# Kernel tuning notes

Measured on AMD Instinct MI355X. Metric: run time of the kernel, lower is better.

Reference implementation:

```python
import jax, jax.numpy as jnp
import numpy as np

ALPHA = 0.2        # LeakyReLU negative slope
OUT_FEATURE = 256
NEG_INF = -1e9


def setup_inputs() -> dict:
    key = jax.random.key(0)
    k1, k2, k3, k4 = jax.random.split(key, 4)
    N, F_IN, F_OUT = 8192, 512, OUT_FEATURE
    x = jax.random.normal(k1, (N, F_IN), dtype=jnp.float32)
    adj = jax.random.randint(k2, (N, N), 0, 2, dtype=jnp.int32)
    # Xavier-uniform-ish params
    W = jax.random.normal(k3, (F_IN, F_OUT), dtype=jnp.float32) * (1.414 / np.sqrt(F_IN))
    a = jax.random.normal(k4, (2 * F_OUT, 1), dtype=jnp.float32) * (1.414 / np.sqrt(2 * F_OUT))
    return {"x": x, "adj": adj, "W": W, "a": a}


def reference(x, adj, W, a):
    # x: [N, F_in], adj: [N, N] int, W: [F_in, F_out], a: [2*F_out, 1]
    h = x @ W                                   # [N, F_out]
    a_src = a[:OUT_FEATURE, 0]                  # [F_out]
    a_dst = a[OUT_FEATURE:, 0]                  # [F_out]
    e_i = h @ a_src                             # [N]
    e_j = h @ a_dst                             # [N]
    e = e_i[:, None] + e_j[None, :]             # [N, N] additive scores
    e = jnp.where(e > 0, e, ALPHA * e)          # LeakyReLU
    e = jnp.where(adj <= 0, NEG_INF, e)         # mask non-edges
    attn = jax.nn.softmax(e, axis=-1)           # row-wise softmax
    out = attn @ h                              # [N, F_out] aggregate
    return jax.nn.elu(out)                      # dropout is identity in eval
```

## Files before the change

### kernel.cpp

```cpp
#include <hip/hip_runtime.h>
#include <hip/hip_fp16.h>

#define N_NODES 8192
#define F_IN    512
#define F_OUT   256
#define LOG2E   1.4426950408889634f

typedef __attribute__((ext_vector_type(8))) _Float16 half8;
typedef __attribute__((ext_vector_type(2))) __fp16   fp16x2;
typedef __attribute__((ext_vector_type(4))) float    f32x4;
typedef __attribute__((ext_vector_type(4))) int      i32x4;

union H8U4 { half8 h; uint4 u; };
union H2U  { fp16x2 h; unsigned u; };

__global__ __launch_bounds__(256) void k_prep(const float* __restrict__ W,
                                              unsigned short* __restrict__ wph,
                                              unsigned short* __restrict__ wpl,
                                              unsigned* __restrict__ emax_u) {
  const int gid = blockIdx.x * 256 + threadIdx.x;
  if (gid == 0) *emax_u = 0u;
  const int k = gid >> 8;
  const int c = gid & 255;
  const float w = W[(size_t)k * F_OUT + c];
  const _Float16 hi = (_Float16)w;
  const _Float16 lo = (_Float16)(w - (float)hi);
  const size_t idx =
      (((size_t)(k >> 5) * 16 + (c >> 4)) * 64 + (c & 15) + 16 * ((k >> 3) & 3)) * 8 +
      (k & 7);
  wph[idx] = *(const unsigned short*)&hi;
  wpl[idx] = *(const unsigned short*)&lo;
}

__global__ __launch_bounds__(512) void k_hgemm(const float* __restrict__ x,
                                               const uint4* __restrict__ wph4,
                                               const uint4* __restrict__ wpl4,
                                               const float* __restrict__ a,
                                               unsigned short* __restrict__ hpack,
                                               float* __restrict__ EI,
                                               float* __restrict__ EJ,
                                               unsigned* __restrict__ emax_u) {
  __shared__ float eip[4][32], ejp[4][32], emx[32];
  const int r0   = blockIdx.x * 32;
  const int tid  = threadIdx.x;
  const int wid  = tid >> 6, lane = tid & 63;
  const int mg   = wid >> 2, ng = wid & 3;
  const int lo16 = lane & 15, hi4 = lane >> 4;

  const float* xrow = x + (size_t)(r0 + mg * 16 + lo16) * F_IN + hi4 * 8;
  const uint4* whb = wph4 + (size_t)(ng * 4) * 64 + lane;
  const uint4* wlb = wpl4 + (size_t)(ng * 4) * 64 + lane;

  f32x4 acc[4] = {};

  float4 xa = *(const float4*)(xrow);
  float4 xb = *(const float4*)(xrow + 4);
  uint4 wh[4], wl[4];
#pragma unroll
  for (int nf = 0; nf < 4; ++nf) {
    wh[nf] = whb[(size_t)nf * 64];
    wl[nf] = wlb[(size_t)nf * 64];
  }

#pragma unroll
  for (int ks = 0; ks < 16; ++ks) {
    H8U4 ah, al;
    const float v[8] = {xa.x, xa.y, xa.z, xa.w, xb.x, xb.y, xb.z, xb.w};
#pragma unroll
    for (int j = 0; j < 8; ++j) {
      const _Float16 h = (_Float16)v[j];
      ah.h[j] = h;
      al.h[j] = (_Float16)(v[j] - (float)h);
    }
    if (ks + 1 < 16) {
      xa = *(const float4*)(xrow + (ks + 1) * 32);
      xb = *(const float4*)(xrow + (ks + 1) * 32 + 4);
    }
#pragma unroll
    for (int nf = 0; nf < 4; ++nf) {
      H8U4 bh, bl;
      bh.u = wh[nf];
      bl.u = wl[nf];
      acc[nf] = __builtin_amdgcn_mfma_f32_16x16x32_f16(ah.h, bh.h, acc[nf], 0, 0, 0);
      acc[nf] = __builtin_amdgcn_mfma_f32_16x16x32_f16(al.h, bh.h, acc[nf], 0, 0, 0);
      acc[nf] = __builtin_amdgcn_mfma_f32_16x16x32_f16(ah.h, bl.h, acc[nf], 0, 0, 0);
    }
    if (ks + 1 < 16) {
#pragma unroll
      for (int nf = 0; nf < 4; ++nf) {
        wh[nf] = whb[(size_t)((ks + 1) * 16 + nf) * 64];
        wl[nf] = wlb[(size_t)((ks + 1) * 16 + nf) * 64];
      }
    }
  }

  float asv[4], adv[4];
#pragma unroll
  for (int nf = 0; nf < 4; ++nf) {
    const int c = ng * 64 + nf * 16 + lo16;
    asv[nf] = a[c];
    adv[nf] = a[F_OUT + c];
  }
#pragma unroll
  for (int q = 0; q < 4; ++q) {
    float s1 = acc[0][q] * asv[0] + acc[1][q] * asv[1] + acc[2][q] * asv[2] +
               acc[3][q] * asv[3];
    float s2 = acc[0][q] * adv[0] + acc[1][q] * adv[1] + acc[2][q] * adv[2] +
               acc[3][q] * adv[3];
#pragma unroll
    for (int o = 1; o < 16; o <<= 1) {
      s1 += __shfl_xor(s1, o);
      s2 += __shfl_xor(s2, o);
    }
    if (lo16 == 0) {
      const int rl = mg * 16 + hi4 * 4 + q;
      eip[ng][rl] = s1;
      ejp[ng][rl] = s2;
    }
  }

#pragma unroll
  for (int nf = 0; nf < 4; ++nf) {
#pragma unroll
    for (int q = 0; q < 4; ++q) {
      const int row = r0 + mg * 16 + hi4 * 4 + q;
      const int col = ng * 64 + nf * 16 + lo16;
      const size_t idx =
          (((size_t)(row >> 5) * 16 + (col >> 4)) * 64 + (col & 15) +
           16 * ((row >> 3) & 3)) * 8 + (row & 7);
      const _Float16 hv = (_Float16)acc[nf][q];
      hpack[idx] = *(const unsigned short*)&hv;
    }
  }

  __syncthreads();
  if (tid < 32) {
    const float s1 = eip[0][tid] + eip[1][tid] + eip[2][tid] + eip[3][tid];
    const float s2 = ejp[0][tid] + ejp[1][tid] + ejp[2][tid] + ejp[3][tid];
    const int row = r0 + tid;
    EI[row] = s1 * LOG2E;
    const float e2 = s2 * LOG2E;
    EJ[row] = e2;
    emx[tid] = e2;
  }
  __syncthreads();
  if (tid == 0) {
    float m = emx[0];
#pragma unroll
    for (int i = 1; i < 32; ++i) m = fmaxf(m, emx[i]);
    unsigned b = __float_as_uint(m);
    unsigned u = (b & 0x80000000u) ? ~b : (b | 0x80000000u);
    atomicMax(emax_u, u);
  }
}

__global__ __launch_bounds__(512, 4) void k_pv(const int* __restrict__ adj,
                                               const uint4* __restrict__ hp4,
                                               const float* __restrict__ EI,
                                               const float* __restrict__ EJ,
                                               const unsigned* __restrict__ emax_u,
                                               float* __restrict__ npart,
                                               float* __restrict__ dpart,
                                               int ntiles) {
  __shared__ __align__(16) uint4 ps4[8 * 64];
  __shared__ float ejhi[2048], ejlo[2048];
  __shared__ float A1[64], A2[64], den[64];
  __shared__ unsigned char bml[2][512];
  const int rowbase = blockIdx.x * 64;
  const int split   = blockIdx.y;
  const int jt0     = split * ntiles;
  const int tid     = threadIdx.x;
  const int wid  = tid >> 6, lane = tid & 63;
  const int lo   = lane & 15, hi = lane >> 4;

  float EMAX;
  {
    const unsigned u = *emax_u;
    EMAX = (u & 0x80000000u) ? __uint_as_float(u & 0x7fffffffu) : __uint_as_float(~u);
  }
  if (tid < 64) {
    const float e  = EI[rowbase + tid];
    const float s  = e + EMAX;
    const float mi = fmaxf(s, 0.2f * s);
    A1[tid] = e - mi;
    A2[tid] = 0.2f * e - mi;
    den[tid] = 0.f;
  }
  const bool uselds = (ntiles <= 32);
  if (uselds) {
    int eidx = jt0 * 64 + tid * 4;
    if (eidx > N_NODES - 4) eidx = N_NODES - 4;
    const float4 ev = *(const float4*)&EJ[eidx];
    *(float4*)&ejhi[tid * 4] = ev;
    float4 el = {0.2f * ev.x, 0.2f * ev.y, 0.2f * ev.z, 0.2f * ev.w};
    *(float4*)&ejlo[tid * 4] = el;
  }

  const int arow = tid >> 3;
  const int* aadj = adj + (size_t)(rowbase + arow) * N_NODES + jt0 * 64 + (tid & 7) * 8;
  {
    const i32x4 v0 = __builtin_nontemporal_load((const i32x4*)(aadj));
    const i32x4 v1 = __builtin_nontemporal_load((const i32x4*)(aadj + 4));
    unsigned by = (v0.x > 0) | ((v0.y > 0) << 1) | ((v0.z > 0) << 2) |
                  ((v0.w > 0) << 3) | ((v1.x > 0) << 4) | ((v1.y > 0) << 5) |
                  ((v1.z > 0) << 6) | ((v1.w > 0) << 7);
    bml[0][tid] = (unsigned char)by;
  }
  i32x4 av0 = {0, 0, 0, 0}, av1 = {0, 0, 0, 0};
  if (ntiles > 1) {
    av0 = __builtin_nontemporal_load((const i32x4*)(aadj + 64));
    av1 = __builtin_nontemporal_load((const i32x4*)(aadj + 68));
  }
  __syncthreads();

  const int msub = wid & 3, ksw = wid >> 2;
  const int row_p = msub * 16 + lo;
  const int jloc  = ksw * 32 + hi * 8;
  const float a1r = A1[row_p], a2r = A2[row_p];
  const int  mbidx = row_p * 8 + ksw * 4 + hi;
  const float* ejg  = EJ + jt0 * 64 + jloc;
  const int mg = wid >> 2, ng = wid & 3;
  const uint4* hb = hp4 + (ng * 4) * 64 + lane;

  f32x4 acc[2][4] = {};
  float dacc = 0.f;

  for (int jt = 0; jt < ntiles; ++jt) {
    const int tb = (jt0 + jt) * 2048;
    const uint4 b00 = hb[tb + 0 * 1024 + 0 * 64];
    const uint4 b01 = hb[tb + 0 * 1024 + 1 * 64];
    const uint4 b02 = hb[tb + 0 * 1024 + 2 * 64];
    const uint4 b03 = hb[tb + 0 * 1024 + 3 * 64];
    const uint4 b10 = hb[tb + 1 * 1024 + 0 * 64];
    const uint4 b11 = hb[tb + 1 * 1024 + 1 * 64];
    const uint4 b12 = hb[tb + 1 * 1024 + 2 * 64];
    const uint4 b13 = hb[tb + 1 * 1024 + 3 * 64];

    const unsigned mcur = bml[jt & 1][mbidx];
    float eh[8], el[8];
    if (uselds) {
      const float4 h0 = *(const float4*)&ejhi[jt * 64 + jloc];
      const float4 h1 = *(const float4*)&ejhi[jt * 64 + jloc + 4];
      const float4 l0 = *(const float4*)&ejlo[jt * 64 + jloc];
      const float4 l1 = *(const float4*)&ejlo[jt * 64 + jloc + 4];
      eh[0]=h0.x; eh[1]=h0.y; eh[2]=h0.z; eh[3]=h0.w;
      eh[4]=h1.x; eh[5]=h1.y; eh[6]=h1.z; eh[7]=h1.w;
      el[0]=l0.x; el[1]=l0.y; el[2]=l0.z; el[3]=l0.w;
      el[4]=l1.x; el[5]=l1.y; el[6]=l1.z; el[7]=l1.w;
    } else {
      const float4 e0 = *(const float4*)(ejg + jt * 64);
      const float4 e1 = *(const float4*)(ejg + jt * 64 + 4);
      eh[0]=e0.x; eh[1]=e0.y; eh[2]=e0.z; eh[3]=e0.w;
      eh[4]=e1.x; eh[5]=e1.y; eh[6]=e1.z; eh[7]=e1.w;
#pragma unroll
      for (int j = 0; j < 8; ++j) el[j] = 0.2f * eh[j];
    }
    float ph[8];
#pragma unroll
    for (int j = 0; j < 8; ++j) {
      const float s = fmaxf(eh[j] + a1r, el[j] + a2r);
      const float p = __builtin_amdgcn_exp2f(s);
      ph[j] = (mcur & (1u << j)) ? p : 0.f;
    }
    dacc += ((ph[0] + ph[1]) + (ph[2] + ph[3])) + ((ph[4] + ph[5]) + (ph[6] + ph[7]));
    H2U q0, q1, q2, q3;
    q0.h = __builtin_amdgcn_cvt_pkrtz(ph[0], ph[1]);
    q1.h = __builtin_amdgcn_cvt_pkrtz(ph[2], ph[3]);
    q2.h = __builtin_amdgcn_cvt_pkrtz(ph[4], ph[5]);
    q3.h = __builtin_amdgcn_cvt_pkrtz(ph[6], ph[7]);
    uint4 pk = {q0.u, q1.u, q2.u, q3.u};

    asm volatile("" ::: "memory");
    __builtin_amdgcn_s_barrier();
    asm volatile("" ::: "memory");
    ps4[wid * 64 + lane] = pk;
    if (jt + 1 < ntiles) {
      unsigned by = (av0.x > 0) | ((av0.y > 0) << 1) | ((av0.z > 0) << 2) |
                    ((av0.w > 0) << 3) | ((av1.x > 0) << 4) | ((av1.y > 0) << 5) |
                    ((av1.z > 0) << 6) | ((av1.w > 0) << 7);
      bml[(jt + 1) & 1][tid] = (unsigned char)by;
      if (jt + 2 < ntiles) {
        av0 = __builtin_nontemporal_load((const i32x4*)(aadj + (jt + 2) * 64));
        av1 = __builtin_nontemporal_load((const i32x4*)(aadj + (jt + 2) * 64 + 4));
      }
    }
    asm volatile("s_waitcnt lgkmcnt(0)" ::: "memory");
    __builtin_amdgcn_s_barrier();
    asm volatile("" ::: "memory");

    H8U4 a00, a01, a10, a11;
    a00.u = ps4[(0 * 4 + mg * 2 + 0) * 64 + lane];
    a10.u = ps4[(0 * 4 + mg * 2 + 1) * 64 + lane];
    a01.u = ps4[(1 * 4 + mg * 2 + 0) * 64 + lane];
    a11.u = ps4[(1 * 4 + mg * 2 + 1) * 64 + lane];
    H8U4 b;
    __builtin_amdgcn_s_setprio(1);
    b.u = b00;
    acc[0][0] = __builtin_amdgcn_mfma_f32_16x16x32_f16(a00.h, b.h, acc[0][0], 0, 0, 0);
    acc[1][0] = __builtin_amdgcn_mfma_f32_16x16x32_f16(a10.h, b.h, acc[1][0], 0, 0, 0);
    b.u = b01;
    acc[0][1] = __builtin_amdgcn_mfma_f32_16x16x32_f16(a00.h, b.h, acc[0][1], 0, 0, 0);
    acc[1][1] = __builtin_amdgcn_mfma_f32_16x16x32_f16(a10.h, b.h, acc[1][1], 0, 0, 0);
    b.u = b02;
    acc[0][2] = __builtin_amdgcn_mfma_f32_16x16x32_f16(a00.h, b.h, acc[0][2], 0, 0, 0);
    acc[1][2] = __builtin_amdgcn_mfma_f32_16x16x32_f16(a10.h, b.h, acc[1][2], 0, 0, 0);
    b.u = b03;
    acc[0][3] = __builtin_amdgcn_mfma_f32_16x16x32_f16(a00.h, b.h, acc[0][3], 0, 0, 0);
    acc[1][3] = __builtin_amdgcn_mfma_f32_16x16x32_f16(a10.h, b.h, acc[1][3], 0, 0, 0);
    b.u = b10;
    acc[0][0] = __builtin_amdgcn_mfma_f32_16x16x32_f16(a01.h, b.h, acc[0][0], 0, 0, 0);
    acc[1][0] = __builtin_amdgcn_mfma_f32_16x16x32_f16(a11.h, b.h, acc[1][0], 0, 0, 0);
    b.u = b11;
    acc[0][1] = __builtin_amdgcn_mfma_f32_16x16x32_f16(a01.h, b.h, acc[0][1], 0, 0, 0);
    acc[1][1] = __builtin_amdgcn_mfma_f32_16x16x32_f16(a11.h, b.h, acc[1][1], 0, 0, 0);
    b.u = b12;
    acc[0][2] = __builtin_amdgcn_mfma_f32_16x16x32_f16(a01.h, b.h, acc[0][2], 0, 0, 0);
    acc[1][2] = __builtin_amdgcn_mfma_f32_16x16x32_f16(a11.h, b.h, acc[1][2], 0, 0, 0);
    b.u = b13;
    acc[0][3] = __builtin_amdgcn_mfma_f32_16x16x32_f16(a01.h, b.h, acc[0][3], 0, 0, 0);
    acc[1][3] = __builtin_amdgcn_mfma_f32_16x16x32_f16(a11.h, b.h, acc[1][3], 0, 0, 0);
    __builtin_amdgcn_s_setprio(0);
  }

  atomicAdd(&den[row_p], dacc);
  __syncthreads();

  float* npb = npart + (size_t)split * N_NODES * F_OUT;
#pragma unroll
  for (int mi_ = 0; mi_ < 2; ++mi_) {
    const int rb = rowbase + (mg * 2 + mi_) * 16 + hi * 4;
#pragma unroll
    for (int nf = 0; nf < 4; ++nf) {
      const int col = ng * 64 + nf * 16 + lo;
#pragma unroll
      for (int r2 = 0; r2 < 4; ++r2)
        __builtin_nontemporal_store(acc[mi_][nf][r2],
                                    &npb[(size_t)(rb + r2) * F_OUT + col]);
    }
  }
  if (tid < 64)
    __builtin_nontemporal_store(den[tid],
                                &dpart[(size_t)split * N_NODES + rowbase + tid]);
}

__global__ __launch_bounds__(256) void k_fin(const float* __restrict__ npart,
                                             const float* __restrict__ dpart,
                                             float* __restrict__ out,
                                             int nsplit) {
  const int gid = blockIdx.x * 256 + threadIdx.x;
  const int row = gid >> 6;
  const int c4  = (gid & 63) << 2;
  f32x4 s = {0.f, 0.f, 0.f, 0.f};
  float d = 0.f;
  for (int sp = 0; sp < nsplit; ++sp) {
    const f32x4 v = __builtin_nontemporal_load(
        (const f32x4*)(npart + ((size_t)sp * N_NODES + row) * F_OUT + c4));
    s += v;
    d += dpart[(size_t)sp * N_NODES + row];
  }
  const float inv = 1.f / d;
  float o[4] = {s.x * inv, s.y * inv, s.z * inv, s.w * inv};
#pragma unroll
  for (int i = 0; i < 4; ++i) o[i] = (o[i] > 0.f) ? o[i] : expm1f(o[i]);
  float4 ov = {o[0], o[1], o[2], o[3]};
  *(float4*)(out + (size_t)row * F_OUT + c4) = ov;
}

extern "C" void kernel_launch(void* const* d_in, const int* in_sizes, int n_in,
                              void* d_out, int out_size, void* d_ws, size_t ws_size,
                              hipStream_t stream) {
  const float* x   = (const float*)d_in[0];
  const int*   adj = (const int*)d_in[1];
  const float* W   = (const float*)d_in[2];
  const float* a   = (const float*)d_in[3];
  float* out = (float*)d_out;
  char*  ws  = (char*)d_ws;

  unsigned short* hpack = (unsigned short*)ws;
  size_t off = (size_t)4 * 1024 * 1024;
  float* EI = (float*)(ws + off); off += (size_t)N_NODES * 4;
  float* EJ = (float*)(ws + off); off += (size_t)N_NODES * 4;
  unsigned* emax_u = (unsigned*)(ws + off); off += 256;
  float* dpart = (float*)(ws + off); off += (size_t)8 * N_NODES * 4;
  unsigned short* wph = (unsigned short*)(ws + off); off += (size_t)F_IN * F_OUT * 2;
  unsigned short* wpl = (unsigned short*)(ws + off); off += (size_t)F_IN * F_OUT * 2;
  float* npart = (float*)(ws + off);

  int nsplit = 4;
  while (nsplit > 1 && off + (size_t)nsplit * N_NODES * F_OUT * 4 > ws_size) nsplit >>= 1;

  k_prep<<<dim3((F_IN * F_OUT) / 256), dim3(256), 0, stream>>>(W, wph, wpl, emax_u);
  k_hgemm<<<dim3(N_NODES / 32), dim3(512), 0, stream>>>(
      x, (const uint4*)wph, (const uint4*)wpl, a, hpack, EI, EJ, emax_u);
  k_pv<<<dim3(128, nsplit), dim3(512), 0, stream>>>(adj, (const uint4*)hpack, EI, EJ,
                                                    emax_u, npart, dpart, 128 / nsplit);
  k_fin<<<dim3(N_NODES * 64 / 256), dim3(256), 0, stream>>>(npart, dpart, out, nsplit);
}
```

Measured before the change: 141.8 us.

## Double k_pv column tile to 128 per iteration, halving barrier count

Each k_pv iteration now processes 128 adjacency columns instead of 64. This halves the number of loop iterations and the two block barriers each one carries. The precomputed 0.2*EJ LDS array is dropped and recomputed inline, and the P staging buffer and mask buffer grow to match. In exchange, each iteration holds more registers for the B fragments and scores, and the second half of the B loads is issued after the barrier, so their latency may be exposed.

```diff
diff --git a/kernel.cpp b/kernel.cpp
--- a/kernel.cpp
+++ b/kernel.cpp
@@ -162,10 +162,10 @@
                                                float* __restrict__ npart,
                                                float* __restrict__ dpart,
                                                int ntiles) {
-  __shared__ __align__(16) uint4 ps4[8 * 64];
-  __shared__ float ejhi[2048], ejlo[2048];
+  __shared__ __align__(16) uint4 ps4[16 * 64];
+  __shared__ float ejhi[2048];
   __shared__ float A1[64], A2[64], den[64];
-  __shared__ unsigned char bml[2][512];
+  __shared__ unsigned char bml[2][1024];
   const int rowbase = blockIdx.x * 64;
   const int split   = blockIdx.y;
   const int jt0     = split * ntiles;
@@ -186,39 +186,44 @@
     A2[tid] = 0.2f * e - mi;
     den[tid] = 0.f;
   }
-  const bool uselds = (ntiles <= 32);
+  const bool uselds = (ntiles <= 16);
   if (uselds) {
-    int eidx = jt0 * 64 + tid * 4;
+    int eidx = jt0 * 128 + tid * 4;
     if (eidx > N_NODES - 4) eidx = N_NODES - 4;
-    const float4 ev = *(const float4*)&EJ[eidx];
-    *(float4*)&ejhi[tid * 4] = ev;
-    float4 el = {0.2f * ev.x, 0.2f * ev.y, 0.2f * ev.z, 0.2f * ev.w};
-    *(float4*)&ejlo[tid * 4] = el;
-  }
-
-  const int arow = tid >> 3;
-  const int* aadj = adj + (size_t)(rowbase + arow) * N_NODES + jt0 * 64 + (tid & 7) * 8;
+    *(float4*)&ejhi[tid * 4] = *(const float4*)&EJ[eidx];
+  }
+
+  const int arow = tid >> 3, ac8 = tid & 7;
+  const int* aadj = adj + (size_t)(rowbase + arow) * N_NODES + jt0 * 128 + ac8 * 16;
   {
     const i32x4 v0 = __builtin_nontemporal_load((const i32x4*)(aadj));
     const i32x4 v1 = __builtin_nontemporal_load((const i32x4*)(aadj + 4));
-    unsigned by = (v0.x > 0) | ((v0.y > 0) << 1) | ((v0.z > 0) << 2) |
-                  ((v0.w > 0) << 3) | ((v1.x > 0) << 4) | ((v1.y > 0) << 5) |
-                  ((v1.z > 0) << 6) | ((v1.w > 0) << 7);
-    bml[0][tid] = (unsigned char)by;
-  }
-  i32x4 av0 = {0, 0, 0, 0}, av1 = {0, 0, 0, 0};
+    const i32x4 v2 = __builtin_nontemporal_load((const i32x4*)(aadj + 8));
+    const i32x4 v3 = __builtin_nontemporal_load((const i32x4*)(aadj + 12));
+    unsigned by0 = (v0.x > 0) | ((v0.y > 0) << 1) | ((v0.z > 0) << 2) |
+                   ((v0.w > 0) << 3) | ((v1.x > 0) << 4) | ((v1.y > 0) << 5) |
+                   ((v1.z > 0) << 6) | ((v1.w > 0) << 7);
+    unsigned by1 = (v2.x > 0) | ((v2.y > 0) << 1) | ((v2.z > 0) << 2) |
+                   ((v2.w > 0) << 3) | ((v3.x > 0) << 4) | ((v3.y > 0) << 5) |
+                   ((v3.z > 0) << 6) | ((v3.w > 0) << 7);
+    *(unsigned short*)&bml[0][arow * 16 + ac8 * 2] =
+        (unsigned short)(by0 | (by1 << 8));
+  }
+  i32x4 av0 = {0,0,0,0}, av1 = {0,0,0,0}, av2 = {0,0,0,0}, av3 = {0,0,0,0};
   if (ntiles > 1) {
-    av0 = __builtin_nontemporal_load((const i32x4*)(aadj + 64));
-    av1 = __builtin_nontemporal_load((const i32x4*)(aadj + 68));
+    av0 = __builtin_nontemporal_load((const i32x4*)(aadj + 128));
+    av1 = __builtin_nontemporal_load((const i32x4*)(aadj + 132));
+    av2 = __builtin_nontemporal_load((const i32x4*)(aadj + 136));
+    av3 = __builtin_nontemporal_load((const i32x4*)(aadj + 140));
   }
   __syncthreads();
 
-  const int msub = wid & 3, ksw = wid >> 2;
+  const int msub = wid & 3, ksw0 = wid >> 2;
   const int row_p = msub * 16 + lo;
-  const int jloc  = ksw * 32 + hi * 8;
+  const int jloc  = ksw0 * 32 + hi * 8;
   const float a1r = A1[row_p], a2r = A2[row_p];
-  const int  mbidx = row_p * 8 + ksw * 4 + hi;
-  const float* ejg  = EJ + jt0 * 64 + jloc;
+  const int  mbidx = row_p * 16 + ksw0 * 4 + hi;
+  const float* ejg = EJ + jt0 * 128 + jloc;
   const int mg = wid >> 2, ng = wid & 3;
   const uint4* hb = hp4 + (ng * 4) * 64 + lane;
 
@@ -226,99 +231,130 @@
   float dacc = 0.f;
 
   for (int jt = 0; jt < ntiles; ++jt) {
-    const int tb = (jt0 + jt) * 2048;
-    const uint4 b00 = hb[tb + 0 * 1024 + 0 * 64];
-    const uint4 b01 = hb[tb + 0 * 1024 + 1 * 64];
-    const uint4 b02 = hb[tb + 0 * 1024 + 2 * 64];
-    const uint4 b03 = hb[tb + 0 * 1024 + 3 * 64];
-    const uint4 b10 = hb[tb + 1 * 1024 + 0 * 64];
-    const uint4 b11 = hb[tb + 1 * 1024 + 1 * 64];
-    const uint4 b12 = hb[tb + 1 * 1024 + 2 * 64];
-    const uint4 b13 = hb[tb + 1 * 1024 + 3 * 64];
-
-    const unsigned mcur = bml[jt & 1][mbidx];
-    float eh[8], el[8];
+    const int tb = (jt0 + jt) * 4096;
+    uint4 b0[4], b1[4];
+#pragma unroll
+    for (int f = 0; f < 4; ++f) {
+      b0[f] = hb[tb + 0 * 1024 + f * 64];
+      b1[f] = hb[tb + 1 * 1024 + f * 64];
+    }
+
+    const unsigned mb0 = bml[jt & 1][mbidx];
+    const unsigned mb1 = bml[jt & 1][mbidx + 8];
+    float eh[16];
     if (uselds) {
-      const float4 h0 = *(const float4*)&ejhi[jt * 64 + jloc];
-      const float4 h1 = *(const float4*)&ejhi[jt * 64 + jloc + 4];
-      const float4 l0 = *(const float4*)&ejlo[jt * 64 + jloc];
-      const float4 l1 = *(const float4*)&ejlo[jt * 64 + jloc + 4];
+      const float4 h0 = *(const float4*)&ejhi[jt * 128 + jloc];
+      const float4 h1 = *(const float4*)&ejhi[jt * 128 + jloc + 4];
+      const float4 h2 = *(const float4*)&ejhi[jt * 128 + jloc + 64];
+      const float4 h3 = *(const float4*)&ejhi[jt * 128 + jloc + 68];
       eh[0]=h0.x; eh[1]=h0.y; eh[2]=h0.z; eh[3]=h0.w;
       eh[4]=h1.x; eh[5]=h1.y; eh[6]=h1.z; eh[7]=h1.w;
-      el[0]=l0.x; el[1]=l0.y; el[2]=l0.z; el[3]=l0.w;
-      el[4]=l1.x; el[5]=l1.y; el[6]=l1.z; el[7]=l1.w;
+      eh[8]=h2.x; eh[9]=h2.y; eh[10]=h2.z; eh[11]=h2.w;
+      eh[12]=h3.x; eh[13]=h3.y; eh[14]=h3.z; eh[15]=h3.w;
     } else {
-      const float4 e0 = *(const float4*)(ejg + jt * 64);
-      const float4 e1 = *(const float4*)(ejg + jt * 64 + 4);
-      eh[0]=e0.x; eh[1]=e0.y; eh[2]=e0.z; eh[3]=e0.w;
-      eh[4]=e1.x; eh[5]=e1.y; eh[6]=e1.z; eh[7]=e1.w;
-#pragma unroll
-      for (int j = 0; j < 8; ++j) el[j] = 0.2f * eh[j];
-    }
-    float ph[8];
+      const float4 h0 = *(const float4*)(ejg + jt * 128);
+      const float4 h1 = *(const float4*)(ejg + jt * 128 + 4);
+      const float4 h2 = *(const float4*)(ejg + jt * 128 + 64);
+      const float4 h3 = *(const float4*)(ejg + jt * 128 + 68);
+      eh[0]=h0.x; eh[1]=h0.y; eh[2]=h0.z; eh[3]=h0.w;
+      eh[4]=h1.x; eh[5]=h1.y; eh[6]=h1.z; eh[7]=h1.w;
+      eh[8]=h2.x; eh[9]=h2.y; eh[10]=h2.z; eh[11]=h2.w;
+      eh[12]=h3.x; eh[13]=h3.y; eh[14]=h3.z; eh[15]=h3.w;
+    }
+    float ph[16];
 #pragma unroll
     for (int j = 0; j < 8; ++j) {
-      const float s = fmaxf(eh[j] + a1r, el[j] + a2r);
+      const float s = fmaxf(eh[j] + a1r, 0.2f * eh[j] + a2r);
       const float p = __builtin_amdgcn_exp2f(s);
-      ph[j] = (mcur & (1u << j)) ? p : 0.f;
-    }
-    dacc += ((ph[0] + ph[1]) + (ph[2] + ph[3])) + ((ph[4] + ph[5]) + (ph[6] + ph[7]));
-    H2U q0, q1, q2, q3;
+      ph[j] = (mb0 & (1u << j)) ? p : 0.f;
+    }
+#pragma unroll
+    for (int j = 8; j < 16; ++j) {
+      const float s = fmaxf(eh[j] + a1r, 0.2f * eh[j] + a2r);
+      const float p = __builtin_amdgcn_exp2f(s);
+      ph[j] = (mb1 & (1u << (j - 8))) ? p : 0.f;
+    }
+#pragma unroll
+    for (int j = 0; j < 16; ++j) dacc += ph[j];
+    H2U q0, q1, q2, q3, q4, q5, q6, q7;
     q0.h = __builtin_amdgcn_cvt_pkrtz(ph[0], ph[1]);
     q1.h = __builtin_amdgcn_cvt_pkrtz(ph[2], ph[3]);
     q2.h = __builtin_amdgcn_cvt_pkrtz(ph[4], ph[5]);
     q3.h = __builtin_amdgcn_cvt_pkrtz(ph[6], ph[7]);
-    uint4 pk = {q0.u, q1.u, q2.u, q3.u};
+    q4.h = __builtin_amdgcn_cvt_pkrtz(ph[8], ph[9]);
+    q5.h = __builtin_amdgcn_cvt_pkrtz(ph[10], ph[11]);
+    q6.h = __builtin_amdgcn_cvt_pkrtz(ph[12], ph[13]);
+    q7.h = __builtin_amdgcn_cvt_pkrtz(ph[14], ph[15]);
+    uint4 pk0 = {q0.u, q1.u, q2.u, q3.u};
+    uint4 pk1 = {q4.u, q5.u, q6.u, q7.u};
 
     asm volatile("" ::: "memory");
     __builtin_amdgcn_s_barrier();
     asm volatile("" ::: "memory");
-    ps4[wid * 64 + lane] = pk;
+    ps4[wid * 64 + lane]       = pk0;
+    ps4[(wid + 8) * 64 + lane] = pk1;
     if (jt + 1 < ntiles) {
-      unsigned by = (av0.x > 0) | ((av0.y > 0) << 1) | ((av0.z > 0) << 2) |
-                    ((av0.w > 0) << 3) | ((av1.x > 0) << 4) | ((av1.y > 0) << 5) |
-                    ((av1.z > 0) << 6) | ((av1.w > 0) << 7);
-      bml[(jt + 1) & 1][tid] = (unsigned char)by;
+      unsigned by0 = (av0.x > 0) | ((av0.y > 0) << 1) | ((av0.z > 0) << 2) |
+                     ((av0.w > 0) << 3) | ((av1.x > 0) << 4) | ((av1.y > 0) << 5) |
+                     ((av1.z > 0) << 6) | ((av1.w > 0) << 7);
+      unsigned by1 = (av2.x > 0) | ((av2.y > 0) << 1) | ((av2.z > 0) << 2) |
+                     ((av2.w > 0) << 3) | ((av3.x > 0) << 4) | ((av3.y > 0) << 5) |
+                     ((av3.z > 0) << 6) | ((av3.w > 0) << 7);
+      *(unsigned short*)&bml[(jt + 1) & 1][arow * 16 + ac8 * 2] =
+          (unsigned short)(by0 | (by1 << 8));
       if (jt + 2 < ntiles) {
-        av0 = __builtin_nontemporal_load((const i32x4*)(aadj + (jt + 2) * 64));
-        av1 = __builtin_nontemporal_load((const i32x4*)(aadj + (jt + 2) * 64 + 4));
+        const int* ap = aadj + (jt + 2) * 128;
+        av0 = __builtin_nontemporal_load((const i32x4*)(ap));
+        av1 = __builtin_nontemporal_load((const i32x4*)(ap + 4));
+        av2 = __builtin_nontemporal_load((const i32x4*)(ap + 8));
+        av3 = __builtin_nontemporal_load((const i32x4*)(ap + 12));
       }
     }
     asm volatile("s_waitcnt lgkmcnt(0)" ::: "memory");
     __builtin_amdgcn_s_barrier();
     asm volatile("" ::: "memory");
 
-    H8U4 a00, a01, a10, a11;
-    a00.u = ps4[(0 * 4 + mg * 2 + 0) * 64 + lane];
-    a10.u = ps4[(0 * 4 + mg * 2 + 1) * 64 + lane];
-    a01.u = ps4[(1 * 4 + mg * 2 + 0) * 64 + lane];
-    a11.u = ps4[(1 * 4 + mg * 2 + 1) * 64 + lane];
-    H8U4 b;
+    uint4 b2[4], b3[4];
+#pragma unroll
+    for (int f = 0; f < 4; ++f) {
+      b2[f] = hb[tb + 2 * 1024 + f * 64];
+      b3[f] = hb[tb + 3 * 1024 + f * 64];
+    }
+
+    H8U4 a0, a1, b;
     __builtin_amdgcn_s_setprio(1);
-    b.u = b00;
-    acc[0][0] = __builtin_amdgcn_mfma_f32_16x16x32_f16(a00.h, b.h, acc[0][0], 0, 0, 0);
-    acc[1][0] = __builtin_amdgcn_mfma_f32_16x16x32_f16(a10.h, b.h, acc[1][0], 0, 0, 0);
-    b.u = b01;
-    acc[0][1] = __builtin_amdgcn_mfma_f32_16x16x32_f16(a00.h, b.h, acc[0][1], 0, 0, 0);
-    acc[1][1] = __builtin_amdgcn_mfma_f32_16x16x32_f16(a10.h, b.h, acc[1][1], 0, 0, 0);
-    b.u = b02;
-    acc[0][2] = __builtin_amdgcn_mfma_f32_16x16x32_f16(a00.h, b.h, acc[0][2], 0, 0, 0);
-    acc[1][2] = __builtin_amdgcn_mfma_f32_16x16x32_f16(a10.h, b.h, acc[1][2], 0, 0, 0);
-    b.u = b03;
-    acc[0][3] = __builtin_amdgcn_mfma_f32_16x16x32_f16(a00.h, b.h, acc[0][3], 0, 0, 0);
-    acc[1][3] = __builtin_amdgcn_mfma_f32_16x16x32_f16(a10.h, b.h, acc[1][3], 0, 0, 0);
-    b.u = b10;
-    acc[0][0] = __builtin_amdgcn_mfma_f32_16x16x32_f16(a01.h, b.h, acc[0][0], 0, 0, 0);
-    acc[1][0] = __builtin_amdgcn_mfma_f32_16x16x32_f16(a11.h, b.h, acc[1][0], 0, 0, 0);
-    b.u = b11;
-    acc[0][1] = __builtin_amdgcn_mfma_f32_16x16x32_f16(a01.h, b.h, acc[0][1], 0, 0, 0);
-    acc[1][1] = __builtin_amdgcn_mfma_f32_16x16x32_f16(a11.h, b.h, acc[1][1], 0, 0, 0);
-    b.u = b12;
-    acc[0][2] = __builtin_amdgcn_mfma_f32_16x16x32_f16(a01.h, b.h, acc[0][2], 0, 0, 0);
-    acc[1][2] = __builtin_amdgcn_mfma_f32_16x16x32_f16(a11.h, b.h, acc[1][2], 0, 0, 0);
-    b.u = b13;
-    acc[0][3] = __builtin_amdgcn_mfma_f32_16x16x32_f16(a01.h, b.h, acc[0][3], 0, 0, 0);
-    acc[1][3] = __builtin_amdgcn_mfma_f32_16x16x32_f16(a11.h, b.h, acc[1][3], 0, 0, 0);
+    a0.u = ps4[(0 * 4 + mg * 2 + 0) * 64 + lane];
+    a1.u = ps4[(0 * 4 + mg * 2 + 1) * 64 + lane];
+#pragma unroll
+    for (int f = 0; f < 4; ++f) {
+      b.u = b0[f];
+      acc[0][f] = __builtin_amdgcn_mfma_f32_16x16x32_f16(a0.h, b.h, acc[0][f], 0, 0, 0);
+      acc[1][f] = __builtin_amdgcn_mfma_f32_16x16x32_f16(a1.h, b.h, acc[1][f], 0, 0, 0);
+    }
+    a0.u = ps4[(1 * 4 + mg * 2 + 0) * 64 + lane];
+    a1.u = ps4[(1 * 4 + mg * 2 + 1) * 64 + lane];
+#pragma unroll
+    for (int f = 0; f < 4; ++f) {
+      b.u = b1[f];
+      acc[0][f] = __builtin_amdgcn_mfma_f32_16x16x32_f16(a0.h, b.h, acc[0][f], 0, 0, 0);
+      acc[1][f] = __builtin_amdgcn_mfma_f32_16x16x32_f16(a1.h, b.h, acc[1][f], 0, 0, 0);
+    }
+    a0.u = ps4[(2 * 4 + mg * 2 + 0) * 64 + lane];
+    a1.u = ps4[(2 * 4 + mg * 2 + 1) * 64 + lane];
+#pragma unroll
+    for (int f = 0; f < 4; ++f) {
+      b.u = b2[f];
+      acc[0][f] = __builtin_amdgcn_mfma_f32_16x16x32_f16(a0.h, b.h, acc[0][f], 0, 0, 0);
+      acc[1][f] = __builtin_amdgcn_mfma_f32_16x16x32_f16(a1.h, b.h, acc[1][f], 0, 0, 0);
+    }
+    a0.u = ps4[(3 * 4 + mg * 2 + 0) * 64 + lane];
+    a1.u = ps4[(3 * 4 + mg * 2 + 1) * 64 + lane];
+#pragma unroll
+    for (int f = 0; f < 4; ++f) {
+      b.u = b3[f];
+      acc[0][f] = __builtin_amdgcn_mfma_f32_16x16x32_f16(a0.h, b.h, acc[0][f], 0, 0, 0);
+      acc[1][f] = __builtin_amdgcn_mfma_f32_16x16x32_f16(a1.h, b.h, acc[1][f], 0, 0, 0);
+    }
     __builtin_amdgcn_s_setprio(0);
   }
 
@@ -393,6 +429,7 @@
   k_hgemm<<<dim3(N_NODES / 32), dim3(512), 0, stream>>>(
       x, (const uint4*)wph, (const uint4*)wpl, a, hpack, EI, EJ, emax_u);
   k_pv<<<dim3(128, nsplit), dim3(512), 0, stream>>>(adj, (const uint4*)hpack, EI, EJ,
-                                                    emax_u, npart, dpart, 128 / nsplit);
+                                                    emax_u, npart, dpart,
+                                                    (N_NODES / 128) / nsplit);
   k_fin<<<dim3(N_NODES * 64 / 256), dim3(256), 0, stream>>>(npart, dpart, out, nsplit);
 }
```

Result: slower. 203.0 us (+43.2%).

## Compute attention probabilities per-wave in registers, dropping LDS exchange and barrier

Applied to the files above, without the earlier changes.

Each wave now computes the exp-score fragments it needs for its own MFMA A operands, instead of splitting the work across waves and exchanging packed probabilities through shared memory. This removes the ps4 LDS buffer, one barrier per tile, and the precomputed ejlo array. In exchange, each probability is recomputed by four waves (one per column group), so exp and VALU work per tile rises about fourfold. The remaining barrier moves to the end of the loop and only protects the mask double buffer.

```diff
diff --git a/kernel.cpp b/kernel.cpp
--- a/kernel.cpp
+++ b/kernel.cpp
@@ -162,8 +162,7 @@
                                                float* __restrict__ npart,
                                                float* __restrict__ dpart,
                                                int ntiles) {
-  __shared__ __align__(16) uint4 ps4[8 * 64];
-  __shared__ float ejhi[2048], ejlo[2048];
+  __shared__ float ejhi[2048];
   __shared__ float A1[64], A2[64], den[64];
   __shared__ unsigned char bml[2][512];
   const int rowbase = blockIdx.x * 64;
@@ -190,10 +189,7 @@
   if (uselds) {
     int eidx = jt0 * 64 + tid * 4;
     if (eidx > N_NODES - 4) eidx = N_NODES - 4;
-    const float4 ev = *(const float4*)&EJ[eidx];
-    *(float4*)&ejhi[tid * 4] = ev;
-    float4 el = {0.2f * ev.x, 0.2f * ev.y, 0.2f * ev.z, 0.2f * ev.w};
-    *(float4*)&ejlo[tid * 4] = el;
+    *(float4*)&ejhi[tid * 4] = *(const float4*)&EJ[eidx];
   }
 
   const int arow = tid >> 3;
@@ -213,17 +209,16 @@
   }
   __syncthreads();
 
-  const int msub = wid & 3, ksw = wid >> 2;
-  const int row_p = msub * 16 + lo;
-  const int jloc  = ksw * 32 + hi * 8;
-  const float a1r = A1[row_p], a2r = A2[row_p];
-  const int  mbidx = row_p * 8 + ksw * 4 + hi;
-  const float* ejg  = EJ + jt0 * 64 + jloc;
   const int mg = wid >> 2, ng = wid & 3;
+  const int r0l = mg * 32 + lo, r1l = r0l + 16;
+  const float a1r0 = A1[r0l], a2r0 = A2[r0l];
+  const float a1r1 = A1[r1l], a2r1 = A2[r1l];
+  const int mb_r0 = r0l * 8, mb_r1 = r1l * 8;
   const uint4* hb = hp4 + (ng * 4) * 64 + lane;
+  const float* ejg = EJ + jt0 * 64;
 
   f32x4 acc[2][4] = {};
-  float dacc = 0.f;
+  float dacc0 = 0.f, dacc1 = 0.f;
 
   for (int jt = 0; jt < ntiles; ++jt) {
     const int tb = (jt0 + jt) * 2048;
@@ -236,63 +231,68 @@
     const uint4 b12 = hb[tb + 1 * 1024 + 2 * 64];
     const uint4 b13 = hb[tb + 1 * 1024 + 3 * 64];
 
-    const unsigned mcur = bml[jt & 1][mbidx];
-    float eh[8], el[8];
+    const unsigned m00 = bml[jt & 1][mb_r0 + hi];
+    const unsigned m01 = bml[jt & 1][mb_r0 + 4 + hi];
+    const unsigned m10 = bml[jt & 1][mb_r1 + hi];
+    const unsigned m11 = bml[jt & 1][mb_r1 + 4 + hi];
+
+    float eh0[8], eh1[8];
     if (uselds) {
-      const float4 h0 = *(const float4*)&ejhi[jt * 64 + jloc];
-      const float4 h1 = *(const float4*)&ejhi[jt * 64 + jloc + 4];
-      const float4 l0 = *(const float4*)&ejlo[jt * 64 + jloc];
-      const float4 l1 = *(const float4*)&ejlo[jt * 64 + jloc + 4];
-      eh[0]=h0.x; eh[1]=h0.y; eh[2]=h0.z; eh[3]=h0.w;
-      eh[4]=h1.x; eh[5]=h1.y; eh[6]=h1.z; eh[7]=h1.w;
-      el[0]=l0.x; el[1]=l0.y; el[2]=l0.z; el[3]=l0.w;
-      el[4]=l1.x; el[5]=l1.y; el[6]=l1.z; el[7]=l1.w;
+      const float4 h0 = *(const float4*)&ejhi[jt * 64 + hi * 8];
+      const float4 h1 = *(const float4*)&ejhi[jt * 64 + hi * 8 + 4];
+      const float4 h2 = *(const float4*)&ejhi[jt * 64 + 32 + hi * 8];
+      const float4 h3 = *(const float4*)&ejhi[jt * 64 + 32 + hi * 8 + 4];
+      eh0[0]=h0.x; eh0[1]=h0.y; eh0[2]=h0.z; eh0[3]=h0.w;
+      eh0[4]=h1.x; eh0[5]=h1.y; eh0[6]=h1.z; eh0[7]=h1.w;
+      eh1[0]=h2.x; eh1[1]=h2.y; eh1[2]=h2.z; eh1[3]=h2.w;
+      eh1[4]=h3.x; eh1[5]=h3.y; eh1[6]=h3.z; eh1[7]=h3.w;
     } else {
-      const float4 e0 = *(const float4*)(ejg + jt * 64);
-      const float4 e1 = *(const float4*)(ejg + jt * 64 + 4);
-      eh[0]=e0.x; eh[1]=e0.y; eh[2]=e0.z; eh[3]=e0.w;
-      eh[4]=e1.x; eh[5]=e1.y; eh[6]=e1.z; eh[7]=e1.w;
-#pragma unroll
-      for (int j = 0; j < 8; ++j) el[j] = 0.2f * eh[j];
-    }
-    float ph[8];
-#pragma unroll
-    for (int j = 0; j < 8; ++j) {
-      const float s = fmaxf(eh[j] + a1r, el[j] + a2r);
-      const float p = __builtin_amdgcn_exp2f(s);
-      ph[j] = (mcur & (1u << j)) ? p : 0.f;
-    }
-    dacc += ((ph[0] + ph[1]) + (ph[2] + ph[3])) + ((ph[4] + ph[5]) + (ph[6] + ph[7]));
-    H2U q0, q1, q2, q3;
-    q0.h = __builtin_amdgcn_cvt_pkrtz(ph[0], ph[1]);
-    q1.h = __builtin_amdgcn_cvt_pkrtz(ph[2], ph[3]);
-    q2.h = __builtin_amdgcn_cvt_pkrtz(ph[4], ph[5]);
-    q3.h = __builtin_amdgcn_cvt_pkrtz(ph[6], ph[7]);
-    uint4 pk = {q0.u, q1.u, q2.u, q3.u};
-
-    asm volatile("" ::: "memory");
-    __builtin_amdgcn_s_barrier();
-    asm volatile("" ::: "memory");
-    ps4[wid * 64 + lane] = pk;
+      const float4 h0 = *(const float4*)(ejg + jt * 64 + hi * 8);
+      const float4 h1 = *(const float4*)(ejg + jt * 64 + hi * 8 + 4);
+      const float4 h2 = *(const float4*)(ejg + jt * 64 + 32 + hi * 8);
+      const float4 h3 = *(const float4*)(ejg + jt * 64 + 32 + hi * 8 + 4);
+      eh0[0]=h0.x; eh0[1]=h0.y; eh0[2]=h0.z; eh0[3]=h0.w;
+      eh0[4]=h1.x; eh0[5]=h1.y; eh0[6]=h1.z; eh0[7]=h1.w;
+      eh1[0]=h2.x; eh1[1]=h2.y; eh1[2]=h2.z; eh1[3]=h2.w;
+      eh1[4]=h3.x; eh1[5]=h3.y; eh1[6]=h3.z; eh1[7]=h3.w;
+    }
+
+    auto mk = [&](const float* eh, unsigned m, float a1, float a2,
+                  float& dac) -> uint4 {
+      float p[8];
+#pragma unroll
+      for (int e = 0; e < 8; ++e) {
+        const float s = fmaxf(eh[e] + a1, 0.2f * eh[e] + a2);
+        const float v = __builtin_amdgcn_exp2f(s);
+        p[e] = (m & (1u << e)) ? v : 0.f;
+      }
+      dac += ((p[0] + p[1]) + (p[2] + p[3])) + ((p[4] + p[5]) + (p[6] + p[7]));
+      H2U q0, q1, q2, q3;
+      q0.h = __builtin_amdgcn_cvt_pkrtz(p[0], p[1]);
+      q1.h = __builtin_amdgcn_cvt_pkrtz(p[2], p[3]);
+      q2.h = __builtin_amdgcn_cvt_pkrtz(p[4], p[5]);
+      q3.h = __builtin_amdgcn_cvt_pkrtz(p[6], p[7]);
+      uint4 r = {q0.u, q1.u, q2.u, q3.u};
+      return r;
+    };
+    H8U4 a00, a10, a01, a11;
+    a00.u = mk(eh0, m00, a1r0, a2r0, dacc0);
+    a10.u = mk(eh0, m10, a1r1, a2r1, dacc1);
+    a01.u = mk(eh1, m01, a1r0, a2r0, dacc0);
+    a11.u = mk(eh1, m11, a1r1, a2r1, dacc1);
+
     if (jt + 1 < ntiles) {
       unsigned by = (av0.x > 0) | ((av0.y > 0) << 1) | ((av0.z > 0) << 2) |
                     ((av0.w > 0) << 3) | ((av1.x > 0) << 4) | ((av1.y > 0) << 5) |
                     ((av1.z > 0) << 6) | ((av1.w > 0) << 7);
       bml[(jt + 1) & 1][tid] = (unsigned char)by;
       if (jt + 2 < ntiles) {
-        av0 = __builtin_nontemporal_load((const i32x4*)(aadj + (jt + 2) * 64));
-        av1 = __builtin_nontemporal_load((const i32x4*)(aadj + (jt + 2) * 64 + 4));
+        const int* ap = aadj + (jt + 2) * 64;
+        av0 = __builtin_nontemporal_load((const i32x4*)ap);
+        av1 = __builtin_nontemporal_load((const i32x4*)(ap + 4));
       }
     }
-    asm volatile("s_waitcnt lgkmcnt(0)" ::: "memory");
-    __builtin_amdgcn_s_barrier();
-    asm volatile("" ::: "memory");
-
-    H8U4 a00, a01, a10, a11;
-    a00.u = ps4[(0 * 4 + mg * 2 + 0) * 64 + lane];
-    a10.u = ps4[(0 * 4 + mg * 2 + 1) * 64 + lane];
-    a01.u = ps4[(1 * 4 + mg * 2 + 0) * 64 + lane];
-    a11.u = ps4[(1 * 4 + mg * 2 + 1) * 64 + lane];
+
     H8U4 b;
     __builtin_amdgcn_s_setprio(1);
     b.u = b00;
@@ -320,9 +320,16 @@
     acc[0][3] = __builtin_amdgcn_mfma_f32_16x16x32_f16(a01.h, b.h, acc[0][3], 0, 0, 0);
     acc[1][3] = __builtin_amdgcn_mfma_f32_16x16x32_f16(a11.h, b.h, acc[1][3], 0, 0, 0);
     __builtin_amdgcn_s_setprio(0);
-  }
-
-  atomicAdd(&den[row_p], dacc);
+
+    asm volatile("s_waitcnt lgkmcnt(0)" ::: "memory");
+    __builtin_amdgcn_s_barrier();
+    asm volatile("" ::: "memory");
+  }
+
+  if (ng == 0) {
+    atomicAdd(&den[r0l], dacc0);
+    atomicAdd(&den[r1l], dacc1);
+  }
   __syncthreads();
 
   float* npb = npart + (size_t)split * N_NODES * F_OUT;
```

Result: slower. 192.0 us (+35.4%).
